# Optimization experiments

Hardware: AMD Instinct MI355X
Metric: run time of the kernel (lower is better)

## Reference

```python
import jax, jax.numpy as jnp
import numpy as np

# Static hyperparams matching init_kwargs
G, D, N, W, KS, AH, AS = 8, 16, 16, 16, 4, 2, 2


def setup_inputs() -> dict:
    key = jax.random.key(0)
    k1, k2 = jax.random.split(key)
    x = jax.random.normal(k1, (8, 128, 32, 1024), dtype=jnp.float32)
    weight = jax.random.normal(k2, (128, 16, 32, 16), dtype=jnp.float32)
    return {"x": x, "weight": weight}


def reference(x, weight):
    b, c, f, T = x.shape
    # pad time axis by w//2 on both sides, then unfold windows of size W, step KS
    xp = jnp.pad(x, ((0, 0), (0, 0), (0, 0), (W // 2, W // 2)))
    t = (xp.shape[-1] - W) // KS + 1
    tidx = jnp.arange(t)[:, None] * KS + jnp.arange(W)[None, :]  # [t, W]
    xw = xp[..., tidx]                                            # [b, c, f, t, W]
    xw = xw.reshape(b, G, D, f, t, W)
    Wg = weight.reshape(G, N, D, f, W)
    # Fused broadcast-multiply + sum over d and w (the all-ones conv sums d and w)
    s = jnp.einsum('bgdftw,gndfw->btgnf', xw, Wg)                 # [b, t, G, N, f]
    s = s.reshape(b, t, G * N, f)
    # box-sum over frequency with window AH, stride AS (fixed all-ones conv height)
    sp = jnp.pad(s, ((0, 0), (0, 0), (0, 0), (AH // 2, AH // 2)))
    f_out = (sp.shape[-1] - AH) // AS + 1
    fidx = jnp.arange(f_out)[:, None] * AS + jnp.arange(AH)[None, :]  # [f_out, AH]
    y = sp[..., fidx].sum(-1)                                     # [b, t, o, f_out]
    y = jax.nn.leaky_relu(y, 0.01)
    return jnp.transpose(y, (0, 2, 3, 1))                         # [b, o, f_out, t]
```

## Files before the change

### kernel.cpp

```cpp
#include <hip/hip_runtime.h>


typedef __attribute__((ext_vector_type(8))) short short8v;
typedef __attribute__((ext_vector_type(4))) float f32x4;

#define TPB 256

static __device__ __forceinline__ short f2bf(float f) {
    unsigned u = __builtin_bit_cast(unsigned, f);
    u += 0x7FFFu + ((u >> 16) & 1u);
    return (short)(u >> 16);
}

__global__ __launch_bounds__(TPB, 4) void lconv5(
    const float* __restrict__ x,
    const float* __restrict__ wt,
    float* __restrict__ out)
{
    __shared__ float xl[4352];
    __shared__ float red[4][16];

    const int fo = blockIdx.x, g = blockIdx.y, b = blockIdx.z;
    const int tid  = threadIdx.x;
    const int lane = tid & 63;
    const int wid  = __builtin_amdgcn_readfirstlane(tid >> 6);
    const int cc = lane & 15;
    const int q  = lane >> 4;

    int fvals[2]; int nf = 0;
    if (2*fo - 1 >= 0) fvals[nf++] = 2*fo - 1;
    if (2*fo < 32)     fvals[nf++] = 2*fo;
    const int f0 = fvals[0];
    const int f1 = (nf > 1) ? fvals[1] : f0;

    const int BG = b*128 + g*16;
    const int wlc = (g*16 + cc)*8192 + (q>>1)*512 + 8*(q&1);
    const int rbase = (q>>1)*1040 + 4*cc + 8*(q&1) + 256*wid;

    auto stage = [&](int f, int d, int slot) {
        const float* src = x + ((size_t)((BG + d)*32 + f))*1024 + tid*4;
        __builtin_amdgcn_global_load_lds(
            (const __attribute__((address_space(1))) void*)src,
            (__attribute__((address_space(3))) void*)&xl[slot*1040 + 8 + tid*4],
            16, 0, 0);
    };

    stage(f0, 0, 0);
    stage(f0, 1, 1);
    if (tid < 64) {
        const int slot = tid >> 4, p = tid & 15;
        xl[slot*1040 + (p < 8 ? p : 1024 + p)] = 0.f;
    }

    f32x4 acc[4];
    #pragma unroll
    for (int t = 0; t < 4; ++t) acc[t] = (f32x4){0.f, 0.f, 0.f, 0.f};

    __syncthreads();

    for (int s = 0; s < nf; ++s) {
        const int f = (s == 0) ? f0 : f1;

        short8v afr[8];
        #pragma unroll
        for (int dp = 0; dp < 8; ++dp) {
            const float* wp = wt + wlc + dp*1024 + f*16;
            const float4 w0 = *(const float4*)wp;
            const float4 w1 = *(const float4*)(wp + 4);
            union { short8v s8; short h[8]; } u;
            u.h[0]=f2bf(w0.x); u.h[1]=f2bf(w0.y); u.h[2]=f2bf(w0.z); u.h[3]=f2bf(w0.w);
            u.h[4]=f2bf(w1.x); u.h[5]=f2bf(w1.y); u.h[6]=f2bf(w1.z); u.h[7]=f2bf(w1.w);
            afr[dp] = u.s8;
        }

        #pragma unroll
        for (int dp = 0; dp < 8; ++dp) {
            const int bi = dp & 1;
            if (!(dp == 7 && s == nf - 1)) {
                const int sn = (dp == 7) ? s + 1 : s;
                const int fn = (sn == 0) ? f0 : f1;
                const int dn = (dp == 7) ? 0 : dp + 1;
                stage(fn, 2*dn,     (bi^1)*2);
                stage(fn, 2*dn + 1, (bi^1)*2 + 1);
            }

            const float* xp = xl + bi*2080 + rbase;
            #pragma unroll
            for (int tt = 0; tt < 4; ++tt) {
                const float4 a0 = *(const float4*)(xp + 64*tt);
                const float4 a1 = *(const float4*)(xp + 64*tt + 4);
                union { short8v s8; short h[8]; } ub;
                ub.h[0]=f2bf(a0.x); ub.h[1]=f2bf(a0.y); ub.h[2]=f2bf(a0.z); ub.h[3]=f2bf(a0.w);
                ub.h[4]=f2bf(a1.x); ub.h[5]=f2bf(a1.y); ub.h[6]=f2bf(a1.z); ub.h[7]=f2bf(a1.w);
                acc[tt] = __builtin_amdgcn_mfma_f32_16x16x32_bf16(
                              afr[dp], ub.s8, acc[tt], 0, 0, 0);
            }
            __syncthreads();
        }
    }

    {
        float* tp = xl + wid*1088;
        #pragma unroll
        for (int tt = 0; tt < 4; ++tt)
            #pragma unroll
            for (int r = 0; r < 4; ++r) {
                float v = acc[tt][r];
                v = (v > 0.f) ? v : 0.01f*v;
                tp[(q*4 + r)*68 + tt*16 + cc] = v;
            }
        #pragma unroll
        for (int p = 0; p < 4; ++p) {
            const int linear = p*64 + lane;
            const int nn = linear >> 4;
            const int c4 = linear & 15;
            const float4 vv = *(const float4*)(tp + nn*68 + c4*4);
            const size_t ob = (size_t)(BG + nn)*4369 + (size_t)fo*257
                            + wid*64 + c4*4;
            out[ob + 0] = vv.x; out[ob + 1] = vv.y;
            out[ob + 2] = vv.z; out[ob + 3] = vv.w;
        }
    }

    {
        const int n = tid & 15;
        const int d = tid >> 4;
        const size_t xrow_bg = (size_t)BG * 32768;
        float p = 0.f;
        for (int s = 0; s < nf; ++s) {
            const int f = (s == 0) ? f0 : f1;
            const float* xr = x + xrow_bg + (size_t)d*32768 + (size_t)f*1024 + 1016;
            const float* wr = wt + (size_t)(g*16 + n)*8192 + (size_t)d*512 + f*16;
            #pragma unroll
            for (int w = 0; w < 8; ++w) p = fmaf(xr[w], wr[w], p);
        }
        p += __shfl_xor(p, 16);
        p += __shfl_xor(p, 32);
        if (lane < 16) red[wid][lane] = p;
        __syncthreads();
        if (tid < 16) {
            float v = red[0][tid] + red[1][tid] + red[2][tid] + red[3][tid];
            v = (v > 0.f) ? v : 0.01f*v;
            out[(size_t)(BG + tid)*4369 + (size_t)fo*257 + 256] = v;
        }
    }
}

extern "C" void kernel_launch(void* const* d_in, const int* in_sizes, int n_in,
                              void* d_out, int out_size, void* d_ws, size_t ws_size,
                              hipStream_t stream) {
    const float* x  = (const float*)d_in[0];
    const float* wt = (const float*)d_in[1];
    float* out      = (float*)d_out;
    dim3 grid(17, 8, 8);
    lconv5<<<grid, TPB, 0, stream>>>(x, wt, out);
}
```

Measured before the change: 53.20 us.

## Deepen LDS staging to four-slot ring with three-ahead prefetch and vmcnt waits

Replaces the double-buffered LDS staging with a four-slot ring buffer and issues async global-to-LDS loads three d-pair steps ahead. Per-step synchronization changes from a full __syncthreads after compute to explicit s_waitcnt vmcnt counts followed by a raw s_barrier before compute. The goal is to keep more global loads in flight and shorten stalls on memory latency. LDS use roughly doubles, which may reduce occupancy, and correctness depends on the hand-set vmcnt counts matching the number of outstanding loads.

After: 54.07 us. No clear change (+1.6%).

```diff
diff --git a/kernel.cpp b/kernel.cpp
--- a/kernel.cpp
+++ b/kernel.cpp
@@ -12,12 +12,12 @@
     return (short)(u >> 16);
 }
 
-__global__ __launch_bounds__(TPB, 4) void lconv5(
+__global__ __launch_bounds__(TPB, 4) void lconv6(
     const float* __restrict__ x,
     const float* __restrict__ wt,
     float* __restrict__ out)
 {
-    __shared__ float xl[4352];
+    __shared__ __attribute__((aligned(16))) float xl[8320];
     __shared__ float red[4][16];
 
     const int fo = blockIdx.x, g = blockIdx.y, b = blockIdx.z;
@@ -25,7 +25,7 @@
     const int lane = tid & 63;
     const int wid  = __builtin_amdgcn_readfirstlane(tid >> 6);
     const int cc = lane & 15;
-    const int q  = lane >> 4;
+    const int kq = lane >> 4;
 
     int fvals[2]; int nf = 0;
     if (2*fo - 1 >= 0) fvals[nf++] = 2*fo - 1;
@@ -34,23 +34,28 @@
     const int f1 = (nf > 1) ? fvals[1] : f0;
 
     const int BG = b*128 + g*16;
-    const int wlc = (g*16 + cc)*8192 + (q>>1)*512 + 8*(q&1);
-    const int rbase = (q>>1)*1040 + 4*cc + 8*(q&1) + 256*wid;
+    const int wlc = (g*16 + cc)*8192 + (kq>>1)*512 + 8*(kq&1);
+    const int rbase = (kq>>1)*1040 + 4*cc + 8*(kq&1) + 256*wid;
 
-    auto stage = [&](int f, int d, int slot) {
-        const float* src = x + ((size_t)((BG + d)*32 + f))*1024 + tid*4;
-        __builtin_amdgcn_global_load_lds(
-            (const __attribute__((address_space(1))) void*)src,
-            (__attribute__((address_space(3))) void*)&xl[slot*1040 + 8 + tid*4],
-            16, 0, 0);
+    auto stage2 = [&](int f_, int dp_, int slot_) {
+        #pragma unroll
+        for (int r = 0; r < 2; ++r) {
+            const float* src = x + ((size_t)((BG + 2*dp_ + r)*32 + f_))*1024 + tid*4;
+            __builtin_amdgcn_global_load_lds(
+                (const __attribute__((address_space(1))) void*)src,
+                (__attribute__((address_space(3))) void*)&xl[slot_*2080 + r*1040 + 8 + tid*4],
+                16, 0, 0);
+        }
     };
 
-    stage(f0, 0, 0);
-    stage(f0, 1, 1);
-    if (tid < 64) {
-        const int slot = tid >> 4, p = tid & 15;
-        xl[slot*1040 + (p < 8 ? p : 1024 + p)] = 0.f;
+    if (tid < 128) {
+        const int row = tid >> 4, p = tid & 15;
+        xl[row*1040 + (p < 8 ? p : 1024 + p)] = 0.f;
     }
+
+    stage2(f0, 0, 0);
+    stage2(f0, 1, 1);
+    stage2(f0, 2, 2);
 
     f32x4 acc[4];
     #pragma unroll
@@ -58,10 +63,11 @@
 
     __syncthreads();
 
+    short8v afr[8];
+
     for (int s = 0; s < nf; ++s) {
         const int f = (s == 0) ? f0 : f1;
 
-        short8v afr[8];
         #pragma unroll
         for (int dp = 0; dp < 8; ++dp) {
             const float* wp = wt + wlc + dp*1024 + f*16;
@@ -73,18 +79,16 @@
             afr[dp] = u.s8;
         }
 
+        const bool tail = (s == nf - 1);
         #pragma unroll
         for (int dp = 0; dp < 8; ++dp) {
-            const int bi = dp & 1;
-            if (!(dp == 7 && s == nf - 1)) {
-                const int sn = (dp == 7) ? s + 1 : s;
-                const int fn = (sn == 0) ? f0 : f1;
-                const int dn = (dp == 7) ? 0 : dp + 1;
-                stage(fn, 2*dn,     (bi^1)*2);
-                stage(fn, 2*dn + 1, (bi^1)*2 + 1);
-            }
+            if (tail && dp == 6)      asm volatile("s_waitcnt vmcnt(2)" ::: "memory");
+            else if (tail && dp == 7) asm volatile("s_waitcnt vmcnt(0)" ::: "memory");
+            else                      asm volatile("s_waitcnt vmcnt(4)" ::: "memory");
+            __builtin_amdgcn_sched_barrier(0);
+            __builtin_amdgcn_s_barrier();
 
-            const float* xp = xl + bi*2080 + rbase;
+            const float* xp = xl + (dp & 3)*2080 + rbase;
             #pragma unroll
             for (int tt = 0; tt < 4; ++tt) {
                 const float4 a0 = *(const float4*)(xp + 64*tt);
@@ -95,9 +99,16 @@
                 acc[tt] = __builtin_amdgcn_mfma_f32_16x16x32_bf16(
                               afr[dp], ub.s8, acc[tt], 0, 0, 0);
             }
-            __syncthreads();
+
+            const int q3 = s*8 + dp + 3;
+            if (q3 < nf*8) {
+                const int f3 = ((q3 >> 3) == 0) ? f0 : f1;
+                stage2(f3, (dp + 3) & 7, (dp + 3) & 3);
+            }
         }
     }
+
+    __syncthreads();
 
     {
         float* tp = xl + wid*1088;
@@ -107,7 +118,7 @@
             for (int r = 0; r < 4; ++r) {
                 float v = acc[tt][r];
                 v = (v > 0.f) ? v : 0.01f*v;
-                tp[(q*4 + r)*68 + tt*16 + cc] = v;
+                tp[(kq*4 + r)*68 + tt*16 + cc] = v;
             }
         #pragma unroll
         for (int p = 0; p < 4; ++p) {
@@ -153,5 +164,5 @@
     const float* wt = (const float*)d_in[1];
     float* out      = (float*)d_out;
     dim3 grid(17, 8, 8);
-    lconv5<<<grid, TPB, 0, stream>>>(x, wt, out);
+    lconv6<<<grid, TPB, 0, stream>>>(x, wt, out);
 }
```

## Replace LDS staging with register double-buffered global loads and patch boundary time steps

Applied to the files above, without the earlier changes.

Drops the global_load_lds double-buffered staging and its per-step __syncthreads. Each lane now loads its x and weight fragments straight from global memory into two register slice buffers, prefetching the next slice while the current one feeds the MFMAs. Boundary time columns (t=0,1,255,256), where the clamped loads give wrong windows, are recomputed with scalar FMAs and patched into LDS before the output is written. Conversion uses packed bf16 intrinsics and launch bounds go from 4 to 3 blocks per SM, trading higher register pressure and redundant global reads for removing barriers.

Result: slower. 55.59 us (+4.5%).

```diff
diff --git a/kernel.cpp b/kernel.cpp
--- a/kernel.cpp
+++ b/kernel.cpp
@@ -1,4 +1,5 @@
 #include <hip/hip_runtime.h>
+#include <hip/hip_bf16.h>
 
 
 typedef __attribute__((ext_vector_type(8))) short short8v;
@@ -6,97 +7,90 @@
 
 #define TPB 256
 
-static __device__ __forceinline__ short f2bf(float f) {
-    unsigned u = __builtin_bit_cast(unsigned, f);
-    u += 0x7FFFu + ((u >> 16) & 1u);
-    return (short)(u >> 16);
+static __device__ __forceinline__ short8v cvt8(const f32x4 a, const f32x4 b) {
+    union { short8v s8; __hip_bfloat162 h2[4]; } u;
+    u.h2[0] = __float22bfloat162_rn(make_float2(a.x, a.y));
+    u.h2[1] = __float22bfloat162_rn(make_float2(a.z, a.w));
+    u.h2[2] = __float22bfloat162_rn(make_float2(b.x, b.y));
+    u.h2[3] = __float22bfloat162_rn(make_float2(b.z, b.w));
+    return u.s8;
 }
 
-__global__ __launch_bounds__(TPB, 4) void lconv5(
+struct SliceBuf {
+    f32x4 xv[4][2];
+    f32x4 wv[2];
+};
+
+__global__ __launch_bounds__(TPB, 3) void lconv13(
     const float* __restrict__ x,
     const float* __restrict__ wt,
     float* __restrict__ out)
 {
-    __shared__ float xl[4352];
-    __shared__ float red[4][16];
+    __shared__ __attribute__((aligned(16))) float xl[4352];
+    __shared__ f32x4 redl[4][16];
 
     const int fo = blockIdx.x, g = blockIdx.y, b = blockIdx.z;
     const int tid  = threadIdx.x;
     const int lane = tid & 63;
     const int wid  = __builtin_amdgcn_readfirstlane(tid >> 6);
     const int cc = lane & 15;
-    const int q  = lane >> 4;
+    const int kq = lane >> 4;
 
-    int fvals[2]; int nf = 0;
-    if (2*fo - 1 >= 0) fvals[nf++] = 2*fo - 1;
-    if (2*fo < 32)     fvals[nf++] = 2*fo;
-    const int f0 = fvals[0];
-    const int f1 = (nf > 1) ? fvals[1] : f0;
+    int f0, f1, nf;
+    if (fo == 0)       { f0 = 0;        f1 = 0;    nf = 1; }
+    else if (fo == 16) { f0 = 31;       f1 = 31;   nf = 1; }
+    else               { f0 = 2*fo - 1; f1 = 2*fo; nf = 2; }
+    const int NS = nf * 8;
 
     const int BG = b*128 + g*16;
-    const int wlc = (g*16 + cc)*8192 + (q>>1)*512 + 8*(q&1);
-    const int rbase = (q>>1)*1040 + 4*cc + 8*(q&1) + 256*wid;
 
-    auto stage = [&](int f, int d, int slot) {
-        const float* src = x + ((size_t)((BG + d)*32 + f))*1024 + tid*4;
-        __builtin_amdgcn_global_load_lds(
-            (const __attribute__((address_space(1))) void*)src,
-            (__attribute__((address_space(3))) void*)&xl[slot*1040 + 8 + tid*4],
-            16, 0, 0);
+    int voffx[4][2];
+    #pragma unroll
+    for (int tt = 0; tt < 4; ++tt) {
+        int tau0 = 64*(4*wid + tt) + 4*cc + 8*(kq & 1) - 8;
+        tau0 = tau0 < 0 ? 0 : (tau0 > 1016 ? 1016 : tau0);
+        voffx[tt][0] = (kq >> 1)*32768 + tau0;
+        voffx[tt][1] = voffx[tt][0] + 4;
+    }
+    const int voffw = cc*8192 + (kq >> 1)*512 + 8*(kq & 1);
+
+    auto issueb = [&](SliceBuf& P, int q_) {
+        const int dp_ = q_ & 7;
+        const int f_  = (q_ >= 8) ? f1 : f0;
+        const float* xb = x + (size_t)(BG + 2*dp_)*32768 + (size_t)f_*1024;
+        const float* wb = wt + (size_t)(g*16)*8192 + (size_t)dp_*1024
+                             + (size_t)f_*16;
+        #pragma unroll
+        for (int tt = 0; tt < 4; ++tt) {
+            P.xv[tt][0] = *(const f32x4*)(xb + voffx[tt][0]);
+            P.xv[tt][1] = *(const f32x4*)(xb + voffx[tt][1]);
+        }
+        P.wv[0] = *(const f32x4*)(wb + voffw);
+        P.wv[1] = *(const f32x4*)(wb + voffw + 4);
     };
-
-    stage(f0, 0, 0);
-    stage(f0, 1, 1);
-    if (tid < 64) {
-        const int slot = tid >> 4, p = tid & 15;
-        xl[slot*1040 + (p < 8 ? p : 1024 + p)] = 0.f;
-    }
 
     f32x4 acc[4];
     #pragma unroll
     for (int t = 0; t < 4; ++t) acc[t] = (f32x4){0.f, 0.f, 0.f, 0.f};
 
-    __syncthreads();
+    auto stepb = [&](SliceBuf& P, int q_, int qn) {
+        const short8v wf = cvt8(P.wv[0], P.wv[1]);
+        short8v xf[4];
+        #pragma unroll
+        for (int tt = 0; tt < 4; ++tt) xf[tt] = cvt8(P.xv[tt][0], P.xv[tt][1]);
+        if (qn < NS) issueb(P, qn);
+        #pragma unroll
+        for (int tt = 0; tt < 4; ++tt)
+            acc[tt] = __builtin_amdgcn_mfma_f32_16x16x32_bf16(
+                          wf, xf[tt], acc[tt], 0, 0, 0);
+    };
 
-    for (int s = 0; s < nf; ++s) {
-        const int f = (s == 0) ? f0 : f1;
-
-        short8v afr[8];
-        #pragma unroll
-        for (int dp = 0; dp < 8; ++dp) {
-            const float* wp = wt + wlc + dp*1024 + f*16;
-            const float4 w0 = *(const float4*)wp;
-            const float4 w1 = *(const float4*)(wp + 4);
-            union { short8v s8; short h[8]; } u;
-            u.h[0]=f2bf(w0.x); u.h[1]=f2bf(w0.y); u.h[2]=f2bf(w0.z); u.h[3]=f2bf(w0.w);
-            u.h[4]=f2bf(w1.x); u.h[5]=f2bf(w1.y); u.h[6]=f2bf(w1.z); u.h[7]=f2bf(w1.w);
-            afr[dp] = u.s8;
-        }
-
-        #pragma unroll
-        for (int dp = 0; dp < 8; ++dp) {
-            const int bi = dp & 1;
-            if (!(dp == 7 && s == nf - 1)) {
-                const int sn = (dp == 7) ? s + 1 : s;
-                const int fn = (sn == 0) ? f0 : f1;
-                const int dn = (dp == 7) ? 0 : dp + 1;
-                stage(fn, 2*dn,     (bi^1)*2);
-                stage(fn, 2*dn + 1, (bi^1)*2 + 1);
-            }
-
-            const float* xp = xl + bi*2080 + rbase;
-            #pragma unroll
-            for (int tt = 0; tt < 4; ++tt) {
-                const float4 a0 = *(const float4*)(xp + 64*tt);
-                const float4 a1 = *(const float4*)(xp + 64*tt + 4);
-                union { short8v s8; short h[8]; } ub;
-                ub.h[0]=f2bf(a0.x); ub.h[1]=f2bf(a0.y); ub.h[2]=f2bf(a0.z); ub.h[3]=f2bf(a0.w);
-                ub.h[4]=f2bf(a1.x); ub.h[5]=f2bf(a1.y); ub.h[6]=f2bf(a1.z); ub.h[7]=f2bf(a1.w);
-                acc[tt] = __builtin_amdgcn_mfma_f32_16x16x32_bf16(
-                              afr[dp], ub.s8, acc[tt], 0, 0, 0);
-            }
-            __syncthreads();
-        }
+    SliceBuf pa, pb;
+    issueb(pa, 0);
+    issueb(pb, 1);
+    for (int q = 0; q < NS; q += 2) {
+        stepb(pa, q,     q + 2);
+        stepb(pb, q + 1, q + 3);
     }
 
     {
@@ -107,8 +101,55 @@
             for (int r = 0; r < 4; ++r) {
                 float v = acc[tt][r];
                 v = (v > 0.f) ? v : 0.01f*v;
-                tp[(q*4 + r)*68 + tt*16 + cc] = v;
+                tp[(kq*4 + r)*68 + tt*16 + cc] = v;
             }
+    }
+    __syncthreads();
+
+    {
+        const int n  = tid & 15;
+        const int dd = tid >> 4;
+        f32x4 p4 = (f32x4){0.f, 0.f, 0.f, 0.f};
+        for (int s = 0; s < nf; ++s) {
+            const int f = (s == 0) ? f0 : f1;
+            const float* xr = x + (size_t)(BG + dd)*32768 + (size_t)f*1024;
+            const float* wr = wt + (size_t)(g*16 + n)*8192 + (size_t)dd*512
+                                 + (size_t)f*16;
+            #pragma unroll
+            for (int w = 0; w < 16; ++w) {
+                const float wv = wr[w];
+                if (w >= 8)  p4.x = fmaf(xr[w - 8],    wv, p4.x);
+                if (w >= 4)  p4.y = fmaf(xr[w - 4],    wv, p4.y);
+                if (w < 12)  p4.z = fmaf(xr[1012 + w], wv, p4.z);
+                if (w < 8)   p4.w = fmaf(xr[1016 + w], wv, p4.w);
+            }
+        }
+        p4.x += __shfl_xor(p4.x, 16); p4.x += __shfl_xor(p4.x, 32);
+        p4.y += __shfl_xor(p4.y, 16); p4.y += __shfl_xor(p4.y, 32);
+        p4.z += __shfl_xor(p4.z, 16); p4.z += __shfl_xor(p4.z, 32);
+        p4.w += __shfl_xor(p4.w, 16); p4.w += __shfl_xor(p4.w, 32);
+        if (lane < 16) redl[wid][lane] = p4;
+    }
+    __syncthreads();
+    if (tid < 16) {
+        f32x4 a = redl[0][tid], bb = redl[1][tid], c = redl[2][tid], d = redl[3][tid];
+        float t0   = a.x + bb.x + c.x + d.x;
+        float t1   = a.y + bb.y + c.y + d.y;
+        float t255 = a.z + bb.z + c.z + d.z;
+        float t256 = a.w + bb.w + c.w + d.w;
+        t0   = (t0   > 0.f) ? t0   : 0.01f*t0;
+        t1   = (t1   > 0.f) ? t1   : 0.01f*t1;
+        t255 = (t255 > 0.f) ? t255 : 0.01f*t255;
+        t256 = (t256 > 0.f) ? t256 : 0.01f*t256;
+        xl[tid*68 + 0] = t0;
+        xl[tid*68 + 1] = t1;
+        xl[3*1088 + tid*68 + 63] = t255;
+        out[(size_t)(BG + tid)*4369 + (size_t)fo*257 + 256] = t256;
+    }
+    __syncthreads();
+
+    {
+        const float* tp = xl + wid*1088;
         #pragma unroll
         for (int p = 0; p < 4; ++p) {
             const int linear = p*64 + lane;
@@ -121,29 +162,6 @@
             out[ob + 2] = vv.z; out[ob + 3] = vv.w;
         }
     }
-
-    {
-        const int n = tid & 15;
-        const int d = tid >> 4;
-        const size_t xrow_bg = (size_t)BG * 32768;
-        float p = 0.f;
-        for (int s = 0; s < nf; ++s) {
-            const int f = (s == 0) ? f0 : f1;
-            const float* xr = x + xrow_bg + (size_t)d*32768 + (size_t)f*1024 + 1016;
-            const float* wr = wt + (size_t)(g*16 + n)*8192 + (size_t)d*512 + f*16;
-            #pragma unroll
-            for (int w = 0; w < 8; ++w) p = fmaf(xr[w], wr[w], p);
-        }
-        p += __shfl_xor(p, 16);
-        p += __shfl_xor(p, 32);
-        if (lane < 16) red[wid][lane] = p;
-        __syncthreads();
-        if (tid < 16) {
-            float v = red[0][tid] + red[1][tid] + red[2][tid] + red[3][tid];
-            v = (v > 0.f) ? v : 0.01f*v;
-            out[(size_t)(BG + tid)*4369 + (size_t)fo*257 + 256] = v;
-        }
-    }
 }
 
 extern "C" void kernel_launch(void* const* d_in, const int* in_sizes, int n_in,
@@ -153,5 +171,5 @@
     const float* wt = (const float*)d_in[1];
     float* out      = (float*)d_out;
     dim3 grid(17, 8, 8);
-    lconv5<<<grid, TPB, 0, stream>>>(x, wt, out);
+    lconv13<<<grid, TPB, 0, stream>>>(x, wt, out);
 }
```
